# Optimization experiments

Measured on AMD Instinct MI355X. Metric: run time of the kernel, lower is better.

The kernel has to match this reference:

```python
import jax, jax.numpy as jnp
import numpy as np
from jax import lax

B, C_IN, C_OUT, K, H, W, NUM = 32, 256, 256, 3, 28, 28, 8


def setup_inputs() -> dict:
    key = jax.random.key(0)
    k1, k2, k3 = jax.random.split(key, 3)
    inputs = jax.random.normal(k1, (B, C_IN, H, W), dtype=jnp.float32)
    inputs_se = jax.random.uniform(k2, (B, NUM), dtype=jnp.float32)
    # weight bank [out*in*k*k, num], init scale sqrt(1/(c*k*k)) as in the module
    scale = np.sqrt(1.0 / (C_IN * K * K)).astype(np.float32)
    weight = jax.random.normal(k3, (C_OUT * C_IN * K * K, NUM), dtype=jnp.float32) * scale
    bias = jnp.zeros((C_OUT,), dtype=jnp.float32)
    return {"inputs": inputs, "inputs_se": inputs_se, "weight": weight, "bias": bias}


def reference(inputs, inputs_se, weight, bias):
    b, c, h, w = inputs.shape
    out_ch = bias.shape[0]
    # per-sample filter generation: [B, num] @ [num, out*in*k*k] -> [B, out, in, k, k]
    wgen = jnp.einsum('bn,on->bo', inputs_se, weight).reshape(b, out_ch, c, K, K)

    def conv_one(x, wk):
        # x: [C,H,W], wk: [O,C,K,K] -> [O,H,W]  (stride 1, padding 1)
        return lax.conv_general_dilated(
            x[None], wk,
            window_strides=(1, 1), padding=[(1, 1), (1, 1)],
            dimension_numbers=('NCHW', 'OIHW', 'NCHW'))[0]

    out = jax.vmap(conv_one)(inputs, wgen)  # [B, O, H, W]
    return out + bias[None, :, None, None]
```

## Files before the change

kernel.cpp:

```cpp
#include <hip/hip_runtime.h>
#include <hip/hip_fp16.h>

#define BB    32
#define CIN   256
#define COUT  256
#define HH    28
#define WW    28
#define NPIX  784
#define HP    30
#define WP    30

#define BM    64
#define BN    128
#define NT    7

#define SLICE_ELEMS 294912
#define WGEN_ELEMS  ((size_t)BB * 2 * SLICE_ELEMS)
#define XPAD_OFF    (WGEN_ELEMS)

#define PREP_GENW  512
#define PREP_GENX  960
#define PREP_GRID  (PREP_GENW + PREP_GENX)

typedef _Float16 f16x8 __attribute__((ext_vector_type(8)));
typedef float    f32x4 __attribute__((ext_vector_type(4)));

static __device__ __forceinline__ ushort f2h_bits(float v) {
    __half h = __float2half(v);
    return *reinterpret_cast<ushort*>(&h);
}

static __device__ __forceinline__ void gll16(const ushort* g, ushort* l) {
    __builtin_amdgcn_global_load_lds(
        (const __attribute__((address_space(1))) unsigned int*)g,
        (__attribute__((address_space(3))) unsigned int*)l, 16, 0, 0);
}

#define KOFF(k) (((k) / 3) * 30 + ((k) % 3))

__global__ __launch_bounds__(256) void prep(const float* __restrict__ weight,
                                            const float* __restrict__ se,
                                            const float* __restrict__ x,
                                            ushort* __restrict__ wgen2,
                                            ushort* __restrict__ xpad) {
    __shared__ __align__(16) char smem[29696];
    const int bid = blockIdx.x;
    const int tid = threadIdx.x;

    if (bid < PREP_GENW) {
        const int og  = bid >> 4;
        const int bh  = (bid >> 3) & 1;
        const int c32 = bid & 7;
        const int ol  = tid >> 5;
        const int cl  = tid & 31;
        const int o   = og * 8 + ol;
        const int c   = c32 * 32 + cl;
        const int mtH = og >> 4;

        float*  se_sh = (float*)smem;
        ushort* w_lds = (ushort*)(smem + 1024);

        se_sh[tid] = se[tid];

        float4 wr[18];
        const float4* wp = (const float4*)(weight + ((size_t)o * CIN + c) * 72);
#pragma unroll
        for (int i = 0; i < 18; ++i) wr[i] = wp[i];

        const int khw0 = tid >> 5;
        const int r0   = tid & 31;
        const int q0   = r0 >> 3;
        const int ol0  = r0 & 7;
        const int o0   = og * 8 + ol0;
        const int sub0 = (o0 >> 4) & 7, col0 = o0 & 15;
        const int dst0 = ((c32 * 9 + khw0) * 512 + sub0 * 64 + q0 * 16 + col0) * 8;
        const int src0 = (khw0 * 8 + ol0) * 40 + q0 * 8;
        const int q1   = tid >> 3;
        const int ol1  = tid & 7;
        const int o1   = og * 8 + ol1;
        const int sub1 = (o1 >> 4) & 7, col1 = o1 & 15;
        const int dst1 = ((c32 * 9 + 8) * 512 + sub1 * 64 + q1 * 16 + col1) * 8;
        const int src1 = (8 * 8 + ol1) * 40 + q1 * 8;

        __syncthreads();

        for (int bi = 0; bi < 16; ++bi) {
            const int b   = bh * 16 + bi;
            const int buf = (bi & 1) * 2880;
            const float s0 = se_sh[b * 8 + 0], s1 = se_sh[b * 8 + 1];
            const float s2 = se_sh[b * 8 + 2], s3 = se_sh[b * 8 + 3];
            const float s4 = se_sh[b * 8 + 4], s5 = se_sh[b * 8 + 5];
            const float s6 = se_sh[b * 8 + 6], s7 = se_sh[b * 8 + 7];
#pragma unroll
            for (int k = 0; k < 9; ++k) {
                const float4 w0 = wr[2 * k + 0];
                const float4 w1 = wr[2 * k + 1];
                const float v = w0.x * s0 + w0.y * s1 + w0.z * s2 + w0.w * s3
                              + w1.x * s4 + w1.y * s5 + w1.z * s6 + w1.w * s7;
                w_lds[buf + (k * 8 + ol) * 40 + cl] = f2h_bits(v);
            }
            __syncthreads();
            ushort* slice_base = wgen2 + (size_t)(b * 2 + mtH) * SLICE_ELEMS;
            *(uint4*)(slice_base + dst0) = *(const uint4*)(w_lds + buf + src0);
            if (tid < 32)
                *(uint4*)(slice_base + dst1) = *(const uint4*)(w_lds + buf + src1);
        }
    } else {
        const int idx = bid - PREP_GENW;
        const int hp  = idx % HP;
        const int b   = idx / HP;
        ushort* row = xpad + ((size_t)b * HP + hp) * WP * CIN;

        if (hp == 0 || hp == HP - 1) {
            uint* r32 = (uint*)row;
            for (int i = tid; i < (WP * CIN) / 2; i += 256) r32[i] = 0u;
            return;
        }
        {
            uint* c0 = (uint*)row;
            uint* c1 = (uint*)(row + (WP - 1) * CIN);
            if (tid < 128)       c0[tid] = 0u;
            else                 c1[tid - 128] = 0u;
        }
        float* lds = (float*)smem;
        const int h = hp - 1;
        const float* xr = x + (size_t)b * CIN * NPIX + h * WW;

        for (int f = tid; f < CIN * WW; f += 256) {
            const int cc = f / WW;
            const int w  = f % WW;
            lds[cc * (WW + 1) + w] = xr[(size_t)cc * NPIX + w];
        }
        __syncthreads();
        for (int g2 = tid; g2 < WW * CIN; g2 += 256) {
            const int w  = g2 >> 8;
            const int cc = g2 & 255;
            row[(w + 1) * CIN + cc] = f2h_bits(lds[cc * (WW + 1) + w]);
        }
    }
}

__global__ __launch_bounds__(256, 4) void dconv_mfma(const ushort* __restrict__ wgen2,
                                                     const ushort* __restrict__ xpad,
                                                     const float* __restrict__ bias,
                                                     float* __restrict__ out) {
    const int bid    = blockIdx.x;
    const int g      = bid & 7;
    const int s      = bid >> 3;
    const int t      = s % 14;
    const int nt     = t % 7;
    const int mtl    = t / 7;
    const int slice2 = g + 8 * (s / 14);
    const int b      = slice2 >> 1;
    const int mtH    = slice2 & 1;

    const int tid  = threadIdx.x;
    const int lane = tid & 63;
    const int wave = tid >> 6;
    const int wm   = wave >> 1;
    const int wn   = wave & 1;
    const int col  = lane & 15;
    const int quad = lane >> 4;

    __shared__ ushort Psh[2][7680];

    const int mo   = mtH * 128 + mtl * 64 + wm * 32;
    const int no   = nt * BN + wn * 64;
    const int h_lo = (nt * BN) / WW;

    const f16x8* ag = (const f16x8*)(wgen2 + (size_t)slice2 * SLICE_ELEMS)
                      + (mtl * 4 + wm * 2) * 64 + lane;
    const ushort* xp = xpad + (size_t)b * HP * WP * CIN;

    int p_goff[4], p_loff[4];
    bool p_ok[4];
#pragma unroll
    for (int r = 0; r < 4; ++r) {
        const int j = r * 256 + tid;
        p_ok[r] = (j < 960);
        const int jj  = p_ok[r] ? j : 0;
        const int qc  = jj / 240;
        const int rem = jj % 240;
        const int rr  = rem / 30;
        const int ww  = rem % 30;
        int srow = h_lo + rr;
        if (srow > 29) srow = 29;
        p_goff[r] = (srow * WP + ww) * CIN + qc * 8;
        p_loff[r] = jj * 8;
    }

    int pixbase[4], pst[4];
#pragma unroll
    for (int j = 0; j < 4; ++j) {
        const int p  = no + j * 16 + col;
        pst[j] = p;
        const int pc = p > (NPIX - 1) ? (NPIX - 1) : p;
        pixbase[j] = (pc / WW - h_lo) * 30 + (pc % WW);
    }

    f32x4 acc[2][4];
#pragma unroll
    for (int mi = 0; mi < 2; ++mi)
#pragma unroll
        for (int nj = 0; nj < 4; ++nj)
            acc[mi][nj] = (f32x4){0.f, 0.f, 0.f, 0.f};

#pragma unroll
    for (int r = 0; r < 4; ++r)
        if (p_ok[r]) gll16(xp + p_goff[r], &Psh[0][p_loff[r]]);

    f16x8 afr[3][2];
#pragma unroll
    for (int mi = 0; mi < 2; ++mi) afr[0][mi] = ag[mi * 64];
    {
        const f16x8* a1 = ag + (1 << 9);
#pragma unroll
        for (int mi = 0; mi < 2; ++mi) afr[1][mi] = a1[mi * 64];
    }

    f16x8 bfr[2][4];

    for (int c32 = 0; c32 < 8; ++c32) {
        __syncthreads();

        if (c32 < 7) {
            const int nb = (c32 + 1) & 1;
#pragma unroll
            for (int r = 0; r < 4; ++r)
                if (p_ok[r]) gll16(xp + p_goff[r] + (c32 + 1) * 32,
                                   &Psh[nb][p_loff[r]]);
        }

        const f16x8* Pc = (const f16x8*)Psh[c32 & 1];

#pragma unroll
        for (int j = 0; j < 4; ++j)
            bfr[0][j] = Pc[quad * 240 + pixbase[j] + KOFF(0)];

#pragma unroll
        for (int khw = 0; khw < 9; ++khw) {
            const int st = c32 * 9 + khw;
            int sp = st + 2; if (sp > 71) sp = 71;
            const f16x8* apf = ag + ((size_t)sp << 9);
#pragma unroll
            for (int mi = 0; mi < 2; ++mi)
                afr[(khw + 2) % 3][mi] = apf[mi * 64];
            if (khw < 8) {
#pragma unroll
                for (int j = 0; j < 4; ++j)
                    bfr[(khw + 1) & 1][j] = Pc[quad * 240 + pixbase[j] + KOFF(khw + 1)];
            }
#pragma unroll
            for (int mi = 0; mi < 2; ++mi)
#pragma unroll
                for (int nj = 0; nj < 4; ++nj)
                    acc[mi][nj] = __builtin_amdgcn_mfma_f32_16x16x32_f16(
                        afr[khw % 3][mi], bfr[khw & 1][nj], acc[mi][nj], 0, 0, 0);
        }
    }

    float* ob = out + (size_t)b * COUT * NPIX;
#pragma unroll
    for (int mi = 0; mi < 2; ++mi) {
        const int m = mo + mi * 16 + quad * 4;
        const float4 bv = *(const float4*)(bias + m);
#pragma unroll
        for (int nj = 0; nj < 4; ++nj) {
            const int p = pst[nj];
            if (p < NPIX) {
                ob[(size_t)(m + 0) * NPIX + p] = acc[mi][nj][0] + bv.x;
                ob[(size_t)(m + 1) * NPIX + p] = acc[mi][nj][1] + bv.y;
                ob[(size_t)(m + 2) * NPIX + p] = acc[mi][nj][2] + bv.z;
                ob[(size_t)(m + 3) * NPIX + p] = acc[mi][nj][3] + bv.w;
            }
        }
    }
}

extern "C" void kernel_launch(void* const* d_in, const int* in_sizes, int n_in,
                              void* d_out, int out_size, void* d_ws, size_t ws_size,
                              hipStream_t stream) {
    const float* x      = (const float*)d_in[0];
    const float* se     = (const float*)d_in[1];
    const float* weight = (const float*)d_in[2];
    const float* bias   = (const float*)d_in[3];
    float* out          = (float*)d_out;

    ushort* wgen2 = (ushort*)d_ws;
    ushort* xpad  = (ushort*)d_ws + XPAD_OFF;
    (void)ws_size; (void)in_sizes; (void)n_in; (void)out_size;

    prep<<<dim3(PREP_GRID), dim3(256), 0, stream>>>(weight, se, x, wgen2, xpad);
    dconv_mfma<<<dim3(BB * 4 * NT), dim3(256), 0, stream>>>(wgen2, xpad, bias, out);
}
```

Measured before the change: 146.5 us.

## Template conv tile on fragment count and deepen B-fragment LDS prefetch

Moves the conv body into a function templated on the number of pixel fragments. The last pixel tile (nt==6) now uses only one 16-pixel fragment instead of four, so it no longer issues MFMAs and LDS reads on padded pixels. The B-fragment LDS reads are also triple-buffered with a two-step-ahead prefetch, which hides LDS latency better but uses more registers. That could hurt occupancy under the launch bounds of 4 blocks per unit.

```diff
diff --git a/kernel.cpp b/kernel.cpp
--- a/kernel.cpp
+++ b/kernel.cpp
@@ -140,6 +140,135 @@
     }
 }
 
+template<int NFR>
+static __device__ __forceinline__ void conv_tile(
+    const ushort* __restrict__ wgen2, const ushort* __restrict__ xpad,
+    const float* __restrict__ bias, float* __restrict__ out,
+    ushort (*Psh)[7680], int b, int mtH, int mtl, int nt, int tid)
+{
+    const int lane = tid & 63;
+    const int wave = tid >> 6;
+    const int wm   = wave >> 1;
+    const int wn   = wave & 1;
+    const int col  = lane & 15;
+    const int quad = lane >> 4;
+
+    const int mo   = mtH * 128 + mtl * 64 + wm * 32;
+    const int no   = nt * BN + wn * 64;
+    const int h_lo = (nt * BN) / WW;
+
+    const f16x8* ag = (const f16x8*)(wgen2 + (size_t)(b * 2 + mtH) * SLICE_ELEMS)
+                      + (mtl * 4 + wm * 2) * 64 + lane;
+    const ushort* xp = xpad + (size_t)b * HP * WP * CIN;
+
+    int p_goff[4], p_loff[4];
+    bool p_ok[4];
+#pragma unroll
+    for (int r = 0; r < 4; ++r) {
+        const int j = r * 256 + tid;
+        p_ok[r] = (j < 960);
+        const int jj  = p_ok[r] ? j : 0;
+        const int qc  = jj / 240;
+        const int rem = jj % 240;
+        const int rr  = rem / 30;
+        const int ww  = rem % 30;
+        int srow = h_lo + rr;
+        if (srow > 29) srow = 29;
+        p_goff[r] = (srow * WP + ww) * CIN + qc * 8;
+        p_loff[r] = jj * 8;
+    }
+
+    int pixbase[NFR], pst[NFR];
+#pragma unroll
+    for (int j = 0; j < NFR; ++j) {
+        const int p  = no + j * 16 + col;
+        pst[j] = p;
+        const int pc = p > (NPIX - 1) ? (NPIX - 1) : p;
+        pixbase[j] = (pc / WW - h_lo) * 30 + (pc % WW);
+    }
+
+    f32x4 acc[2][NFR];
+#pragma unroll
+    for (int mi = 0; mi < 2; ++mi)
+#pragma unroll
+        for (int nj = 0; nj < NFR; ++nj)
+            acc[mi][nj] = (f32x4){0.f, 0.f, 0.f, 0.f};
+
+#pragma unroll
+    for (int r = 0; r < 4; ++r)
+        if (p_ok[r]) gll16(xp + p_goff[r], &Psh[0][p_loff[r]]);
+
+    f16x8 afr[3][2];
+#pragma unroll
+    for (int mi = 0; mi < 2; ++mi) afr[0][mi] = ag[mi * 64];
+    {
+        const f16x8* a1 = ag + (1 << 9);
+#pragma unroll
+        for (int mi = 0; mi < 2; ++mi) afr[1][mi] = a1[mi * 64];
+    }
+
+    f16x8 bfr[3][NFR];
+
+    for (int c32 = 0; c32 < 8; ++c32) {
+        __syncthreads();
+
+        if (c32 < 7) {
+            const int nb = (c32 + 1) & 1;
+#pragma unroll
+            for (int r = 0; r < 4; ++r)
+                if (p_ok[r]) gll16(xp + p_goff[r] + (c32 + 1) * 32,
+                                   &Psh[nb][p_loff[r]]);
+        }
+
+        const f16x8* Pc = (const f16x8*)Psh[c32 & 1];
+
+#pragma unroll
+        for (int j = 0; j < NFR; ++j) {
+            bfr[0][j] = Pc[quad * 240 + pixbase[j] + KOFF(0)];
+            bfr[1][j] = Pc[quad * 240 + pixbase[j] + KOFF(1)];
+        }
+
+#pragma unroll
+        for (int khw = 0; khw < 9; ++khw) {
+            const int st = c32 * 9 + khw;
+            int sp = st + 2; if (sp > 71) sp = 71;
+            const f16x8* apf = ag + ((size_t)sp << 9);
+#pragma unroll
+            for (int mi = 0; mi < 2; ++mi)
+                afr[(khw + 2) % 3][mi] = apf[mi * 64];
+            if (khw < 7) {
+#pragma unroll
+                for (int j = 0; j < NFR; ++j)
+                    bfr[(khw + 2) % 3][j] =
+                        Pc[quad * 240 + pixbase[j] + KOFF(khw + 2)];
+            }
+#pragma unroll
+            for (int mi = 0; mi < 2; ++mi)
+#pragma unroll
+                for (int nj = 0; nj < NFR; ++nj)
+                    acc[mi][nj] = __builtin_amdgcn_mfma_f32_16x16x32_f16(
+                        afr[khw % 3][mi], bfr[khw % 3][nj], acc[mi][nj], 0, 0, 0);
+        }
+    }
+
+    float* ob = out + (size_t)b * COUT * NPIX;
+#pragma unroll
+    for (int mi = 0; mi < 2; ++mi) {
+        const int m = mo + mi * 16 + quad * 4;
+        const float4 bv = *(const float4*)(bias + m);
+#pragma unroll
+        for (int nj = 0; nj < NFR; ++nj) {
+            const int p = pst[nj];
+            if (p < NPIX) {
+                ob[(size_t)(m + 0) * NPIX + p] = acc[mi][nj][0] + bv.x;
+                ob[(size_t)(m + 1) * NPIX + p] = acc[mi][nj][1] + bv.y;
+                ob[(size_t)(m + 2) * NPIX + p] = acc[mi][nj][2] + bv.z;
+                ob[(size_t)(m + 3) * NPIX + p] = acc[mi][nj][3] + bv.w;
+            }
+        }
+    }
+}
+
 __global__ __launch_bounds__(256, 4) void dconv_mfma(const ushort* __restrict__ wgen2,
                                                      const ushort* __restrict__ xpad,
                                                      const float* __restrict__ bias,
@@ -153,128 +282,14 @@
     const int slice2 = g + 8 * (s / 14);
     const int b      = slice2 >> 1;
     const int mtH    = slice2 & 1;
-
-    const int tid  = threadIdx.x;
-    const int lane = tid & 63;
-    const int wave = tid >> 6;
-    const int wm   = wave >> 1;
-    const int wn   = wave & 1;
-    const int col  = lane & 15;
-    const int quad = lane >> 4;
+    const int tid    = threadIdx.x;
 
     __shared__ ushort Psh[2][7680];
 
-    const int mo   = mtH * 128 + mtl * 64 + wm * 32;
-    const int no   = nt * BN + wn * 64;
-    const int h_lo = (nt * BN) / WW;
-
-    const f16x8* ag = (const f16x8*)(wgen2 + (size_t)slice2 * SLICE_ELEMS)
-                      + (mtl * 4 + wm * 2) * 64 + lane;
-    const ushort* xp = xpad + (size_t)b * HP * WP * CIN;
-
-    int p_goff[4], p_loff[4];
-    bool p_ok[4];
-#pragma unroll
-    for (int r = 0; r < 4; ++r) {
-        const int j = r * 256 + tid;
-        p_ok[r] = (j < 960);
-        const int jj  = p_ok[r] ? j : 0;
-        const int qc  = jj / 240;
-        const int rem = jj % 240;
-        const int rr  = rem / 30;
-        const int ww  = rem % 30;
-        int srow = h_lo + rr;
-        if (srow > 29) srow = 29;
-        p_goff[r] = (srow * WP + ww) * CIN + qc * 8;
-        p_loff[r] = jj * 8;
-    }
-
-    int pixbase[4], pst[4];
-#pragma unroll
-    for (int j = 0; j < 4; ++j) {
-        const int p  = no + j * 16 + col;
-        pst[j] = p;
-        const int pc = p > (NPIX - 1) ? (NPIX - 1) : p;
-        pixbase[j] = (pc / WW - h_lo) * 30 + (pc % WW);
-    }
-
-    f32x4 acc[2][4];
-#pragma unroll
-    for (int mi = 0; mi < 2; ++mi)
-#pragma unroll
-        for (int nj = 0; nj < 4; ++nj)
-            acc[mi][nj] = (f32x4){0.f, 0.f, 0.f, 0.f};
-
-#pragma unroll
-    for (int r = 0; r < 4; ++r)
-        if (p_ok[r]) gll16(xp + p_goff[r], &Psh[0][p_loff[r]]);
-
-    f16x8 afr[3][2];
-#pragma unroll
-    for (int mi = 0; mi < 2; ++mi) afr[0][mi] = ag[mi * 64];
-    {
-        const f16x8* a1 = ag + (1 << 9);
-#pragma unroll
-        for (int mi = 0; mi < 2; ++mi) afr[1][mi] = a1[mi * 64];
-    }
-
-    f16x8 bfr[2][4];
-
-    for (int c32 = 0; c32 < 8; ++c32) {
-        __syncthreads();
-
-        if (c32 < 7) {
-            const int nb = (c32 + 1) & 1;
-#pragma unroll
-            for (int r = 0; r < 4; ++r)
-                if (p_ok[r]) gll16(xp + p_goff[r] + (c32 + 1) * 32,
-                                   &Psh[nb][p_loff[r]]);
-        }
-
-        const f16x8* Pc = (const f16x8*)Psh[c32 & 1];
-
-#pragma unroll
-        for (int j = 0; j < 4; ++j)
-            bfr[0][j] = Pc[quad * 240 + pixbase[j] + KOFF(0)];
-
-#pragma unroll
-        for (int khw = 0; khw < 9; ++khw) {
-            const int st = c32 * 9 + khw;
-            int sp = st + 2; if (sp > 71) sp = 71;
-            const f16x8* apf = ag + ((size_t)sp << 9);
-#pragma unroll
-            for (int mi = 0; mi < 2; ++mi)
-                afr[(khw + 2) % 3][mi] = apf[mi * 64];
-            if (khw < 8) {
-#pragma unroll
-                for (int j = 0; j < 4; ++j)
-                    bfr[(khw + 1) & 1][j] = Pc[quad * 240 + pixbase[j] + KOFF(khw + 1)];
-            }
-#pragma unroll
-            for (int mi = 0; mi < 2; ++mi)
-#pragma unroll
-                for (int nj = 0; nj < 4; ++nj)
-                    acc[mi][nj] = __builtin_amdgcn_mfma_f32_16x16x32_f16(
-                        afr[khw % 3][mi], bfr[khw & 1][nj], acc[mi][nj], 0, 0, 0);
-        }
-    }
-
-    float* ob = out + (size_t)b * COUT * NPIX;
-#pragma unroll
-    for (int mi = 0; mi < 2; ++mi) {
-        const int m = mo + mi * 16 + quad * 4;
-        const float4 bv = *(const float4*)(bias + m);
-#pragma unroll
-        for (int nj = 0; nj < 4; ++nj) {
-            const int p = pst[nj];
-            if (p < NPIX) {
-                ob[(size_t)(m + 0) * NPIX + p] = acc[mi][nj][0] + bv.x;
-                ob[(size_t)(m + 1) * NPIX + p] = acc[mi][nj][1] + bv.y;
-                ob[(size_t)(m + 2) * NPIX + p] = acc[mi][nj][2] + bv.z;
-                ob[(size_t)(m + 3) * NPIX + p] = acc[mi][nj][3] + bv.w;
-            }
-        }
-    }
+    if (nt == 6)
+        conv_tile<1>(wgen2, xpad, bias, out, Psh, b, mtH, mtl, nt, tid);
+    else
+        conv_tile<4>(wgen2, xpad, bias, out, Psh, b, mtH, mtl, nt, tid);
 }
 
 extern "C" void kernel_launch(void* const* d_in, const int* in_sizes, int n_in,
```

Result: no change. 146.1 us (-0.2%).
